# Optimization experiments

Measured on AMD Instinct MI355X. Metric: run time of the kernel, lower is better.

Reference implementation:

```python
import math
import jax, jax.numpy as jnp
import numpy as np

B = 2
IN_DIM = 512
OUT_DIM = 256
MAX_IN_SEQ = 1024
MAX_OUT_SEQ = 512
SEQ = 1024  # actual_seq_len == max_in_seq
LN_EPS = 1e-5
TWO_PI = 2.0 * math.pi


def setup_inputs() -> dict:
    key = jax.random.key(0)
    ks = jax.random.split(key, 4)
    x = jax.random.normal(ks[0], (B * SEQ, IN_DIM), dtype=jnp.float32)
    M = jax.random.uniform(ks[1], (OUT_DIM, IN_DIM), minval=-0.5, maxval=0.5, dtype=jnp.float32)
    P = jax.random.uniform(ks[2], (OUT_DIM, OUT_DIM), minval=-0.1, maxval=0.1, dtype=jnp.float32)
    Linker = jax.random.uniform(ks[3], (MAX_IN_SEQ, MAX_OUT_SEQ), minval=-0.1, maxval=0.1, dtype=jnp.float32)
    ln_gamma = jnp.ones((OUT_DIM,), dtype=jnp.float32)
    ln_beta = jnp.zeros((OUT_DIM,), dtype=jnp.float32)
    return {"x": x, "M": M, "P": P, "Linker": Linker,
            "ln_gamma": ln_gamma, "ln_beta": ln_beta, "actual_seq_len": SEQ}


def _periods(out_dim):
    # periods[i, j] = i * out_dim + j + 2
    i = jnp.arange(out_dim, dtype=jnp.float32)[:, None]
    j = jnp.arange(out_dim, dtype=jnp.float32)[None, :]
    return i * out_dim + j + 2.0


def _layernorm(z, gamma, beta):
    mu = jnp.mean(z, axis=-1, keepdims=True)
    var = jnp.mean(jnp.square(z - mu), axis=-1, keepdims=True)
    return (z - mu) * jax.lax.rsqrt(var + LN_EPS) * gamma + beta


def reference(x, M, P, Linker, ln_gamma, ln_beta, actual_seq_len):
    total, _ = x.shape                      # (B*S, in_dim)
    batch = total // actual_seq_len
    out_seq = max(1, actual_seq_len // 2)   # reduction_factor = 2

    # projection + LayerNorm
    Z = x @ M.T                             # (B*S, out_dim)
    Zn = _layernorm(Z, ln_gamma, ln_beta)

    # position-dependent cos-weighted transform over the flattened B*S axis
    periods = _periods(OUT_DIM)             # (O, O)
    k = jnp.arange(total, dtype=jnp.float32)  # (B*S,)
    phi = jnp.cos(TWO_PI * k[:, None, None] / periods[None])  # (B*S, O, O)
    T = jnp.einsum('kj,ij,kij->ki', Zn, P, phi)               # (B*S, O)

    # adaptive sequence-length reduction via Linker
    AL = Linker[:actual_seq_len, :out_seq]  # (S, S')
    T3 = T.reshape(batch, actual_seq_len, OUT_DIM)
    U = jnp.einsum('bso,st->bto', T3, AL).reshape(batch * out_seq, OUT_DIM)

    # shared residual: reuse M and Linker on the pre-LN projection
    R3 = Z.reshape(batch, actual_seq_len, OUT_DIM)
    R = jnp.einsum('bso,st->bto', R3, AL).reshape(batch * out_seq, OUT_DIM)

    return U + R, out_seq
```

## Files before the change

kernel.cpp:

```cpp
#include <hip/hip_runtime.h>
#include <hip/hip_bf16.h>

#define TOT     2048
#define INDIM   512
#define OD      256
#define SEQL    1024
#define TQ      512
#define NB      2
#define LN_EPS  1e-5f

#define JSPL    16
#define JW      (OD / JSPL)
#define K3SPL   8

typedef __attribute__((ext_vector_type(8))) short bf16x8;
typedef __attribute__((ext_vector_type(4))) float f32x4;
typedef __attribute__((ext_vector_type(2))) float f32x2;

__device__ __forceinline__ short f2bf(float f) {
    __hip_bfloat16 h = __float2bfloat16(f);
    return *(short*)&h;
}
__device__ __forceinline__ uint pack2(float a, float b) {
    return (uint)(ushort)f2bf(a) | ((uint)(ushort)f2bf(b) << 16);
}

__global__ __launch_bounds__(256) void kcvt(
    const float* __restrict__ x, const float* __restrict__ M,
    const float* __restrict__ L,
    short* __restrict__ xb, short* __restrict__ Mb, short* __restrict__ ALt)
{
    const int bid = blockIdx.x;
    const int tid = threadIdx.x;
    if (bid < 1024) {
        const int i = (bid * 256 + tid) * 4;
        float4 v = *(const float4*)(x + i);
        *(uint2*)(xb + i) = make_uint2(pack2(v.x, v.y), pack2(v.z, v.w));
    } else if (bid < 1152) {
        const int i = ((bid - 1024) * 256 + tid) * 4;
        float4 v = *(const float4*)(M + i);
        *(uint2*)(Mb + i) = make_uint2(pack2(v.x, v.y), pack2(v.z, v.w));
    } else {
        __shared__ float tl[32][36];
        const int tt = bid - 1152;
        const int s0 = (tt >> 4) * 32;
        const int t0 = (tt & 15) * 32;
        const int r  = tid >> 3;
        const int c4 = (tid & 7) * 4;
        float4 v = *(const float4*)(L + (size_t)(s0 + r) * TQ + t0 + c4);
        tl[r][c4 + 0] = v.x; tl[r][c4 + 1] = v.y;
        tl[r][c4 + 2] = v.z; tl[r][c4 + 3] = v.w;
        __syncthreads();
        uint lo = pack2(tl[c4 + 0][r], tl[c4 + 1][r]);
        uint hi = pack2(tl[c4 + 2][r], tl[c4 + 3][r]);
        *(uint2*)(ALt + (size_t)(t0 + r) * SEQL + s0 + c4) = make_uint2(lo, hi);
    }
}

__device__ __forceinline__ void mfma_tile64(
    const short* __restrict__ A, int lda,
    const short* __restrict__ B, int ldb,
    float* __restrict__ C, int ldc,
    int r0, int c0, int k0, int nk)
{
    __shared__ short Al[64][40];
    __shared__ short Bl[64][40];
    const int tid = threadIdx.x;
    const int w   = tid >> 6;
    const int wm  = w >> 1, wn = w & 1;
    const int l   = tid & 63;
    const int lr  = l & 15, lg = l >> 4;
    const int srow = tid >> 2, skg = (tid & 3) * 8;

    f32x4 acc[2][2] = {{{0.f,0.f,0.f,0.f},{0.f,0.f,0.f,0.f}},
                       {{0.f,0.f,0.f,0.f},{0.f,0.f,0.f,0.f}}};

    for (int ks = 0; ks < nk; ++ks) {
        const int kb = k0 + ks * 32;
        __syncthreads();
        *(bf16x8*)&Al[srow][skg] = *(const bf16x8*)(A + (size_t)(r0 + srow) * lda + kb + skg);
        *(bf16x8*)&Bl[srow][skg] = *(const bf16x8*)(B + (size_t)(c0 + srow) * ldb + kb + skg);
        __syncthreads();
        bf16x8 a0 = *(const bf16x8*)&Al[wm * 32 +      lr][lg * 8];
        bf16x8 a1 = *(const bf16x8*)&Al[wm * 32 + 16 + lr][lg * 8];
        bf16x8 b0 = *(const bf16x8*)&Bl[wn * 32 +      lr][lg * 8];
        bf16x8 b1 = *(const bf16x8*)&Bl[wn * 32 + 16 + lr][lg * 8];
        acc[0][0] = __builtin_amdgcn_mfma_f32_16x16x32_bf16(a0, b0, acc[0][0], 0, 0, 0);
        acc[0][1] = __builtin_amdgcn_mfma_f32_16x16x32_bf16(a0, b1, acc[0][1], 0, 0, 0);
        acc[1][0] = __builtin_amdgcn_mfma_f32_16x16x32_bf16(a1, b0, acc[1][0], 0, 0, 0);
        acc[1][1] = __builtin_amdgcn_mfma_f32_16x16x32_bf16(a1, b1, acc[1][1], 0, 0, 0);
    }
#pragma unroll
    for (int sm = 0; sm < 2; ++sm)
#pragma unroll
    for (int sn = 0; sn < 2; ++sn)
#pragma unroll
    for (int q = 0; q < 4; ++q)
        C[(size_t)(r0 + wm * 32 + sm * 16 + 4 * lg + q) * ldc
          + (c0 + wn * 32 + sn * 16 + lr)] = acc[sm][sn][q];
}

__global__ __launch_bounds__(256, 4) void k1_mfma(
    const short* __restrict__ xb, const short* __restrict__ Mb,
    float* __restrict__ Zp)
{
    mfma_tile64(xb, INDIM, Mb, INDIM,
                Zp + (size_t)blockIdx.z * TOT * OD, OD,
                blockIdx.x * 64, blockIdx.y * 64, blockIdx.z * 256, 8);
}

__global__ __launch_bounds__(256) void k1b_ln(
    const float* __restrict__ Zp,
    const float* __restrict__ gamma, const float* __restrict__ beta,
    float* __restrict__ Z, float* __restrict__ Zn)
{
    const int r0 = blockIdx.x * 8;
    const int c  = threadIdx.x;

    float acc[8];
#pragma unroll
    for (int r = 0; r < 8; ++r) {
        const size_t i = (size_t)(r0 + r) * OD + c;
        acc[r] = Zp[i] + Zp[(size_t)TOT * OD + i];
    }

    __shared__ float s1[8][4], s2[8][4];
    const int lane = c & 63;
    const int wid  = c >> 6;
#pragma unroll
    for (int r = 0; r < 8; ++r) {
        float s = acc[r], q = acc[r] * acc[r];
#pragma unroll
        for (int off = 32; off > 0; off >>= 1) {
            s += __shfl_xor(s, off, 64);
            q += __shfl_xor(q, off, 64);
        }
        if (lane == 0) { s1[r][wid] = s; s2[r][wid] = q; }
    }
    __syncthreads();
#pragma unroll
    for (int r = 0; r < 8; ++r) {
        float s  = s1[r][0] + s1[r][1] + s1[r][2] + s1[r][3];
        float q  = s2[r][0] + s2[r][1] + s2[r][2] + s2[r][3];
        float mu = s * (1.f / OD);
        float var = q * (1.f / OD) - mu * mu;
        float inv = rsqrtf(var + LN_EPS);
        float z  = acc[r];
        float zn = (z - mu) * inv * gamma[c] + beta[c];
        Z [(size_t)(r0 + r) * OD + c] = z;
        Zn[(size_t)(r0 + r) * OD + c] = zn;
    }
}

__global__ __launch_bounds__(64) void k2_t(
    const float* __restrict__ Zn, const float* __restrict__ P,
    short* __restrict__ Tp)
{
    const int k0 = blockIdx.x * 64;
    const int i0 = blockIdx.y * 32;
    const int j0 = blockIdx.z * JW;

    __shared__ float znT[JW][68];
    __shared__ float pt[32][20];

    const int tid = threadIdx.x;
    {
        const float* zr = Zn + (size_t)(k0 + tid) * OD + j0;
        float4 v0 = *(const float4*)(zr);
        float4 v1 = *(const float4*)(zr + 4);
        float4 v2 = *(const float4*)(zr + 8);
        float4 v3 = *(const float4*)(zr + 12);
        znT[ 0][tid] = v0.x; znT[ 1][tid] = v0.y; znT[ 2][tid] = v0.z; znT[ 3][tid] = v0.w;
        znT[ 4][tid] = v1.x; znT[ 5][tid] = v1.y; znT[ 6][tid] = v1.z; znT[ 7][tid] = v1.w;
        znT[ 8][tid] = v2.x; znT[ 9][tid] = v2.y; znT[10][tid] = v2.z; znT[11][tid] = v2.w;
        znT[12][tid] = v3.x; znT[13][tid] = v3.y; znT[14][tid] = v3.z; znT[15][tid] = v3.w;
        if (tid < 32) {
            const float* pr = P + (size_t)(i0 + tid) * OD + j0;
            *(float4*)&pt[tid][ 0] = *(const float4*)(pr);
            *(float4*)&pt[tid][ 4] = *(const float4*)(pr + 4);
            *(float4*)&pt[tid][ 8] = *(const float4*)(pr + 8);
            *(float4*)&pt[tid][12] = *(const float4*)(pr + 12);
        }
    }
    __syncthreads();

    const int kg = tid & 1;
    const int li = tid >> 1;
    const float kbase = (float)(k0 + kg * 32);
    const float pb0   = (float)((i0 + li) * OD + j0 + 2);

    f32x2 acc[16];
#pragma unroll
    for (int m = 0; m < 16; ++m) acc[m] = (f32x2){0.f, 0.f};

    const float* zrow = &znT[0][kg * 32];

    for (int j = 0; j < JW; ++j) {
        const float p  = pb0 + (float)j;
        const float ip = __builtin_amdgcn_rcpf(p);
        const float a0 = __builtin_amdgcn_fractf(kbase * ip);
        const float c0 = __builtin_amdgcn_cosf(a0);
        const float s0 = __builtin_amdgcn_sinf(a0);
        const float cd = __builtin_amdgcn_cosf(ip);
        const float sd = __builtin_amdgcn_sinf(ip);
        const float c1 = c0 * cd - s0 * sd;
        const float s1 = s0 * cd + c0 * sd;
        const float c2d = 1.f - 2.f * sd * sd;
        const float s2d = 2.f * sd * cd;

        f32x2 C = {c0, c1}, S = {s0, s1};
        const f32x2 C2 = {c2d, c2d}, S2 = {s2d, s2d};
        const float pm = pt[li][j];
        const f32x2 PM = {pm, pm};
        const float* zc = zrow + (size_t)j * 68;

#pragma unroll
        for (int m8 = 0; m8 < 8; ++m8) {
            float4 z4 = *(const float4*)(zc + 4 * m8);
            f32x2 za = {z4.x, z4.y};
            f32x2 zb = {z4.z, z4.w};
            f32x2 t = za * PM;
            acc[2 * m8] = t * C + acc[2 * m8];
            f32x2 Cn = C * C2 - S * S2;
            f32x2 Sn = S * C2 + C * S2;
            C = Cn; S = Sn;
            t = zb * PM;
            acc[2 * m8 + 1] = t * C + acc[2 * m8 + 1];
            Cn = C * C2 - S * S2;
            Sn = S * C2 + C * S2;
            C = Cn; S = Sn;
        }
    }

    short* Tpl = Tp + (size_t)blockIdx.z * (TOT * OD);
    const int ib = i0 + li;
    const int kb = k0 + kg * 32;
#pragma unroll
    for (int m = 0; m < 16; ++m) {
        Tpl[(size_t)(kb + 2 * m    ) * OD + ib] = f2bf(acc[m].x);
        Tpl[(size_t)(kb + 2 * m + 1) * OD + ib] = f2bf(acc[m].y);
    }
}

__global__ __launch_bounds__(256) void k2b_w(
    const float* __restrict__ Z, const short* __restrict__ Tp,
    short* __restrict__ Wt)
{
    __shared__ float tl[32][36];
    const int kt0 = blockIdx.x * 32;
    const int o0  = blockIdx.y * 32;
    const int tid = threadIdx.x;
    const int r   = tid >> 3;
    const int c4  = (tid & 7) * 4;

    const size_t idx = (size_t)(kt0 + r) * OD + o0 + c4;
    float4 z = *(const float4*)(Z + idx);
#pragma unroll
    for (int p = 0; p < JSPL; ++p) {
        uint2 t = *(const uint2*)(Tp + (size_t)p * (TOT * OD) + idx);
        z.x += __uint_as_float(t.x << 16);
        z.y += __uint_as_float(t.x & 0xFFFF0000u);
        z.z += __uint_as_float(t.y << 16);
        z.w += __uint_as_float(t.y & 0xFFFF0000u);
    }
    *(float4*)&tl[r][c4] = z;
    __syncthreads();

    const int ol = tid >> 3;
    const int sc = (tid & 7) * 4;
    const int b  = kt0 >> 10;
    const int sb = kt0 & 1023;
    uint lo = pack2(tl[sc + 0][ol], tl[sc + 1][ol]);
    uint hi = pack2(tl[sc + 2][ol], tl[sc + 3][ol]);
    *(uint2*)(Wt + ((size_t)b * OD + o0 + ol) * SEQL + sb + sc) = make_uint2(lo, hi);
}

__global__ __launch_bounds__(256, 4) void k3_mfma(
    const short* __restrict__ ALt, const short* __restrict__ Wt,
    float* __restrict__ Op)
{
    const int b   = blockIdx.z & 1;
    const int ksp = blockIdx.z >> 1;
    mfma_tile64(ALt, SEQL, Wt + (size_t)b * OD * SEQL, SEQL,
                Op + (size_t)ksp * (NB * TQ * OD) + (size_t)b * TQ * OD, OD,
                blockIdx.x * 64, blockIdx.y * 64, ksp * (SEQL / K3SPL), (SEQL / K3SPL) / 32);
}

__global__ __launch_bounds__(256) void k4_comb(
    const float* __restrict__ Op, float* __restrict__ out, int out_size)
{
    const int m = blockIdx.x * 256 + threadIdx.x;
    const int N4 = (NB * TQ * OD) / 4;
    if (m < N4) {
        float4 a = ((const float4*)Op)[m];
#pragma unroll
        for (int p = 1; p < K3SPL; ++p) {
            float4 t = ((const float4*)(Op + (size_t)p * (NB * TQ * OD)))[m];
            a.x += t.x; a.y += t.y; a.z += t.z; a.w += t.w;
        }
        ((float4*)out)[m] = a;
    }
    if (m == 0 && out_size > NB * TQ * OD)
        out[NB * TQ * OD] = (float)TQ;
}

extern "C" void kernel_launch(void* const* d_in, const int* in_sizes, int n_in,
                              void* d_out, int out_size, void* d_ws, size_t ws_size,
                              hipStream_t stream)
{
    const float* x  = (const float*)d_in[0];
    const float* M  = (const float*)d_in[1];
    const float* P  = (const float*)d_in[2];
    const float* L  = (const float*)d_in[3];
    const float* g  = (const float*)d_in[4];
    const float* be = (const float*)d_in[5];
    float* out = (float*)d_out;

    float* ws_f = (float*)d_ws;
    float* Zp = ws_f;
    float* Z  = Zp + 2 * (size_t)TOT * OD;
    float* Zn = Z  + (size_t)TOT * OD;
    float* Op = Zn + (size_t)TOT * OD;
    short* xb  = (short*)(Op + (size_t)K3SPL * NB * TQ * OD);
    short* Mb  = xb  + (size_t)TOT * INDIM;
    short* ALt = Mb  + (size_t)OD * INDIM;
    short* Wt  = ALt + (size_t)TQ * SEQL;
    short* Tp  = Wt  + (size_t)NB * OD * SEQL;

    kcvt<<<1664, 256, 0, stream>>>(x, M, L, xb, Mb, ALt);
    k1_mfma<<<dim3(TOT / 64, OD / 64, 2), 256, 0, stream>>>(xb, Mb, Zp);
    k1b_ln<<<TOT / 8, 256, 0, stream>>>(Zp, g, be, Z, Zn);
    k2_t<<<dim3(TOT / 64, OD / 32, JSPL), 64, 0, stream>>>(Zn, P, Tp);
    k2b_w<<<dim3(TOT / 32, OD / 32), 256, 0, stream>>>(Z, Tp, Wt);
    k3_mfma<<<dim3(TQ / 64, OD / 64, NB * K3SPL), 256, 0, stream>>>(ALt, Wt, Op);
    k4_comb<<<(NB * TQ * OD / 4 + 255) / 256, 256, 0, stream>>>(Op, out, out_size);
}
```

Measured before the change: 53.95 us.

## Use Chebyshev cosine recurrence and compute two output rows per thread in k2_t

Replaces the rotation-based cos/sin recurrence with a three-term Chebyshev recurrence, cos((n+2)x) = 2cos(2x)·cos(nx) − cos((n−2)x), with the P weight folded into the recurrence state. This cuts the per-element arithmetic in the inner loop. Each thread now handles two adjacent output rows i, so every LDS load of Zn serves both rows. The two bf16 results are written together as one packed 32-bit store. Blocks grow to 128 threads with a transposed P tile in shared memory. The costs are more accumulator registers and possibly slightly more rounding error from the three-term recurrence.

```diff
diff --git a/kernel.cpp b/kernel.cpp
--- a/kernel.cpp
+++ b/kernel.cpp
@@ -152,93 +152,109 @@
     }
 }
 
-__global__ __launch_bounds__(64) void k2_t(
+__global__ __launch_bounds__(128) void k2_t(
     const float* __restrict__ Zn, const float* __restrict__ P,
     short* __restrict__ Tp)
 {
     const int k0 = blockIdx.x * 64;
-    const int i0 = blockIdx.y * 32;
+    const int i0 = blockIdx.y * 128;
     const int j0 = blockIdx.z * JW;
 
     __shared__ float znT[JW][68];
-    __shared__ float pt[32][20];
+    __shared__ float ptT[JW][132];
 
     const int tid = threadIdx.x;
     {
-        const float* zr = Zn + (size_t)(k0 + tid) * OD + j0;
+        const int row = tid & 63;
+        const int jh  = (tid >> 6) * 8;
+        const float* zr = Zn + (size_t)(k0 + row) * OD + j0 + jh;
         float4 v0 = *(const float4*)(zr);
         float4 v1 = *(const float4*)(zr + 4);
-        float4 v2 = *(const float4*)(zr + 8);
-        float4 v3 = *(const float4*)(zr + 12);
-        znT[ 0][tid] = v0.x; znT[ 1][tid] = v0.y; znT[ 2][tid] = v0.z; znT[ 3][tid] = v0.w;
-        znT[ 4][tid] = v1.x; znT[ 5][tid] = v1.y; znT[ 6][tid] = v1.z; znT[ 7][tid] = v1.w;
-        znT[ 8][tid] = v2.x; znT[ 9][tid] = v2.y; znT[10][tid] = v2.z; znT[11][tid] = v2.w;
-        znT[12][tid] = v3.x; znT[13][tid] = v3.y; znT[14][tid] = v3.z; znT[15][tid] = v3.w;
-        if (tid < 32) {
-            const float* pr = P + (size_t)(i0 + tid) * OD + j0;
-            *(float4*)&pt[tid][ 0] = *(const float4*)(pr);
-            *(float4*)&pt[tid][ 4] = *(const float4*)(pr + 4);
-            *(float4*)&pt[tid][ 8] = *(const float4*)(pr + 8);
-            *(float4*)&pt[tid][12] = *(const float4*)(pr + 12);
+        znT[jh + 0][row] = v0.x; znT[jh + 1][row] = v0.y;
+        znT[jh + 2][row] = v0.z; znT[jh + 3][row] = v0.w;
+        znT[jh + 4][row] = v1.x; znT[jh + 5][row] = v1.y;
+        znT[jh + 6][row] = v1.z; znT[jh + 7][row] = v1.w;
+        const float* pr = P + (size_t)(i0 + tid) * OD + j0;
+        float4 p0 = *(const float4*)(pr);
+        float4 p1 = *(const float4*)(pr + 4);
+        float4 p2 = *(const float4*)(pr + 8);
+        float4 p3 = *(const float4*)(pr + 12);
+        ptT[ 0][tid] = p0.x; ptT[ 1][tid] = p0.y; ptT[ 2][tid] = p0.z; ptT[ 3][tid] = p0.w;
+        ptT[ 4][tid] = p1.x; ptT[ 5][tid] = p1.y; ptT[ 6][tid] = p1.z; ptT[ 7][tid] = p1.w;
+        ptT[ 8][tid] = p2.x; ptT[ 9][tid] = p2.y; ptT[10][tid] = p2.z; ptT[11][tid] = p2.w;
+        ptT[12][tid] = p3.x; ptT[13][tid] = p3.y; ptT[14][tid] = p3.z; ptT[15][tid] = p3.w;
+    }
+    __syncthreads();
+
+    const int kg = tid >> 6;
+    const int l  = tid & 63;
+    const int il = 2 * l;
+    const float kbase = (float)(k0 + kg * 32);
+    const float pbA   = (float)((i0 + il) * OD + j0 + 2);
+
+    f32x2 accA[16], accB[16];
+#pragma unroll
+    for (int m = 0; m < 16; ++m) { accA[m] = (f32x2){0.f, 0.f}; accB[m] = (f32x2){0.f, 0.f}; }
+
+    const float* zrow = &znT[0][kg * 32];
+
+    for (int j = 0; j < JW; ++j) {
+        f32x2 wp = *(const f32x2*)&ptT[j][il];
+        const float pA  = pbA + (float)j;
+        const float ipA = __builtin_amdgcn_rcpf(pA);
+        const float aA  = __builtin_amdgcn_fractf(kbase * ipA);
+        const float c0A = __builtin_amdgcn_cosf(aA);
+        const float s0A = __builtin_amdgcn_sinf(aA);
+        const float cdA = __builtin_amdgcn_cosf(ipA);
+        const float sdA = __builtin_amdgcn_sinf(ipA);
+        const float c1A = c0A * cdA - s0A * sdA;
+        const float s1A = s0A * cdA + c0A * sdA;
+        const float c2A = c1A * cdA - s1A * sdA;
+        const float c3A = c2A * cdA - (s1A * cdA + c1A * sdA) * sdA;
+        const float r2A = 2.f * (1.f - 2.f * sdA * sdA);
+        f32x2 DA_p = {wp.x * c0A, wp.x * c1A};
+        f32x2 DA_c = {wp.x * c2A, wp.x * c3A};
+        const f32x2 RA = {r2A, r2A};
+        const float pB  = pA + 256.f;
+        const float ipB = __builtin_amdgcn_rcpf(pB);
+        const float aB  = __builtin_amdgcn_fractf(kbase * ipB);
+        const float c0B = __builtin_amdgcn_cosf(aB);
+        const float s0B = __builtin_amdgcn_sinf(aB);
+        const float cdB = __builtin_amdgcn_cosf(ipB);
+        const float sdB = __builtin_amdgcn_sinf(ipB);
+        const float c1B = c0B * cdB - s0B * sdB;
+        const float s1B = s0B * cdB + c0B * sdB;
+        const float c2B = c1B * cdB - s1B * sdB;
+        const float c3B = c2B * cdB - (s1B * cdB + c1B * sdB) * sdB;
+        const float r2B = 2.f * (1.f - 2.f * sdB * sdB);
+        f32x2 DB_p = {wp.y * c0B, wp.y * c1B};
+        f32x2 DB_c = {wp.y * c2B, wp.y * c3B};
+        const f32x2 RB = {r2B, r2B};
+
+        const float* zc = zrow + (size_t)j * 68;
+#pragma unroll
+        for (int m = 0; m < 8; ++m) {
+            float4 z4 = *(const float4*)(zc + 4 * m);
+            f32x2 zlo = {z4.x, z4.y};
+            f32x2 zhi = {z4.z, z4.w};
+            accA[2 * m    ] += zlo * DA_p;
+            accB[2 * m    ] += zlo * DB_p;
+            f32x2 tA = RA * DA_c - DA_p;  DA_p = DA_c;  DA_c = tA;
+            f32x2 tB = RB * DB_c - DB_p;  DB_p = DB_c;  DB_c = tB;
+            accA[2 * m + 1] += zhi * DA_p;
+            accB[2 * m + 1] += zhi * DB_p;
+            tA = RA * DA_c - DA_p;  DA_p = DA_c;  DA_c = tA;
+            tB = RB * DB_c - DB_p;  DB_p = DB_c;  DB_c = tB;
         }
     }
-    __syncthreads();
-
-    const int kg = tid & 1;
-    const int li = tid >> 1;
-    const float kbase = (float)(k0 + kg * 32);
-    const float pb0   = (float)((i0 + li) * OD + j0 + 2);
-
-    f32x2 acc[16];
-#pragma unroll
-    for (int m = 0; m < 16; ++m) acc[m] = (f32x2){0.f, 0.f};
-
-    const float* zrow = &znT[0][kg * 32];
-
-    for (int j = 0; j < JW; ++j) {
-        const float p  = pb0 + (float)j;
-        const float ip = __builtin_amdgcn_rcpf(p);
-        const float a0 = __builtin_amdgcn_fractf(kbase * ip);
-        const float c0 = __builtin_amdgcn_cosf(a0);
-        const float s0 = __builtin_amdgcn_sinf(a0);
-        const float cd = __builtin_amdgcn_cosf(ip);
-        const float sd = __builtin_amdgcn_sinf(ip);
-        const float c1 = c0 * cd - s0 * sd;
-        const float s1 = s0 * cd + c0 * sd;
-        const float c2d = 1.f - 2.f * sd * sd;
-        const float s2d = 2.f * sd * cd;
-
-        f32x2 C = {c0, c1}, S = {s0, s1};
-        const f32x2 C2 = {c2d, c2d}, S2 = {s2d, s2d};
-        const float pm = pt[li][j];
-        const f32x2 PM = {pm, pm};
-        const float* zc = zrow + (size_t)j * 68;
-
-#pragma unroll
-        for (int m8 = 0; m8 < 8; ++m8) {
-            float4 z4 = *(const float4*)(zc + 4 * m8);
-            f32x2 za = {z4.x, z4.y};
-            f32x2 zb = {z4.z, z4.w};
-            f32x2 t = za * PM;
-            acc[2 * m8] = t * C + acc[2 * m8];
-            f32x2 Cn = C * C2 - S * S2;
-            f32x2 Sn = S * C2 + C * S2;
-            C = Cn; S = Sn;
-            t = zb * PM;
-            acc[2 * m8 + 1] = t * C + acc[2 * m8 + 1];
-            Cn = C * C2 - S * S2;
-            Sn = S * C2 + C * S2;
-            C = Cn; S = Sn;
-        }
-    }
 
     short* Tpl = Tp + (size_t)blockIdx.z * (TOT * OD);
-    const int ib = i0 + li;
+    const int ia = i0 + il;
     const int kb = k0 + kg * 32;
 #pragma unroll
     for (int m = 0; m < 16; ++m) {
-        Tpl[(size_t)(kb + 2 * m    ) * OD + ib] = f2bf(acc[m].x);
-        Tpl[(size_t)(kb + 2 * m + 1) * OD + ib] = f2bf(acc[m].y);
+        *(uint*)(Tpl + (size_t)(kb + 2 * m    ) * OD + ia) = pack2(accA[m].x, accB[m].x);
+        *(uint*)(Tpl + (size_t)(kb + 2 * m + 1) * OD + ia) = pack2(accA[m].y, accB[m].y);
     }
 }
 
@@ -330,7 +346,7 @@
     kcvt<<<1664, 256, 0, stream>>>(x, M, L, xb, Mb, ALt);
     k1_mfma<<<dim3(TOT / 64, OD / 64, 2), 256, 0, stream>>>(xb, Mb, Zp);
     k1b_ln<<<TOT / 8, 256, 0, stream>>>(Zp, g, be, Z, Zn);
-    k2_t<<<dim3(TOT / 64, OD / 32, JSPL), 64, 0, stream>>>(Zn, P, Tp);
+    k2_t<<<dim3(TOT / 64, OD / 128, JSPL), 128, 0, stream>>>(Zn, P, Tp);
     k2b_w<<<dim3(TOT / 32, OD / 32), 256, 0, stream>>>(Z, Tp, Wt);
     k3_mfma<<<dim3(TQ / 64, OD / 64, NB * K3SPL), 256, 0, stream>>>(ALt, Wt, Op);
     k4_comb<<<(NB * TQ * OD / 4 + 255) / 256, 256, 0, stream>>>(Op, out, out_size);
```

Result: faster. 47.39 us (-12.2%).
